# Optimization experiments

Measured on AMD Instinct MI355X. Metric: run time of the kernel, lower is better.

Reference implementation:

```python
import jax, jax.numpy as jnp
import numpy as np

N_QUBITS = 18
BATCH = 8
LAYERS = 4


def setup_inputs() -> dict:
    key = jax.random.key(0)
    k1, k2 = jax.random.split(key)
    batch_betas = jax.random.normal(k1, (BATCH, LAYERS), dtype=jnp.float32)
    adj_matrices = jax.random.uniform(k2, (BATCH, N_QUBITS, N_QUBITS), dtype=jnp.float32)
    return {"batch_betas": batch_betas, "adj_matrices": adj_matrices}


def reference(batch_betas, adj_matrices):
    B, P = batch_betas.shape
    N = adj_matrices.shape[-1]
    dim = 2 ** N

    # Z_i diagonal for qubit i: ones(2^i) kron [1,-1] kron ones(2^(N-1-i)),
    # i.e. z_i(x) = 1 - 2 * bit_{N-1-i}(x).
    idx = jnp.arange(dim)
    shifts = (N - 1 - jnp.arange(N))[:, None]
    Z = 1.0 - 2.0 * ((idx[None, :] >> shifts) & 1).astype(jnp.float32)  # [N, dim]

    # MaxCut diagonal: sum over upper-triangular edges of 0.5 * (1 - z_u * z_v)
    W = (jnp.triu(adj_matrices, k=1) > 0.5).astype(jnp.float32)  # [B, N, N]
    n_edges = jnp.sum(W, axis=(1, 2))                            # [B]
    T = jnp.einsum('buv,vd->bud', W, Z)                          # [B, N, dim]
    cross = jnp.einsum('bud,ud->bd', T, Z)                       # sum_{u<v} W z_u z_v
    hp_diag = 0.5 * (n_edges[:, None] - cross)                   # [B, dim]

    # uniform superposition
    state = jnp.full((B, dim), 1.0 / np.sqrt(dim), dtype=jnp.complex64)
    phase = jnp.exp(-1j * hp_diag)  # e^{-i * H_P * 1.0}, complex64

    for t in range(P):
        state = state * phase
        beta = batch_betas[:, t]
        c = jnp.cos(beta).astype(jnp.complex64)[:, None, None]
        ms = (-1j * jnp.sin(beta).astype(jnp.complex64))[:, None, None]
        # apply RX-like mixer [[c, -i s], [-i s, c]] to each qubit
        for i in range(N):
            s4 = state.reshape(B, 2 ** i, 2, -1)
            s0 = s4[:, :, 0, :]
            s1 = s4[:, :, 1, :]
            new0 = c * s0 + ms * s1
            new1 = ms * s0 + c * s1
            state = jnp.stack([new0, new1], axis=2).reshape(B, dim)

    probs = jnp.abs(state) ** 2
    energy = jnp.sum(probs * hp_diag, axis=1)  # [B]
    return energy
```

## Files before the change

### kernel.cpp

```cpp
#include <hip/hip_runtime.h>
#include <hip/hip_fp16.h>

#define NQ 18
#define QDIM (1 << NQ)
#define NB 8
#define NL 4

typedef unsigned u32;
typedef unsigned long long u64;

#define DPP_XOR1 0xB1
#define DPP_XOR2 0x4E

__device__ __forceinline__ void tbfly(float2& a, float2& b, float t) {
  float nax = fmaf(t, b.y, a.x);
  float nay = fmaf(-t, b.x, a.y);
  float nbx = fmaf(t, a.y, b.x);
  float nby = fmaf(-t, a.x, b.y);
  a = make_float2(nax, nay); b = make_float2(nbx, nby);
}
__device__ __forceinline__ void tstage(float2* v, int m, float t) {
#pragma unroll
  for (int i = 0; i < 16; ++i)
    if (!(i & m)) tbfly(v[i], v[i | m], t);
}
template <int CTRL>
__device__ __forceinline__ void dppstage(float2* v, float t) {
#pragma unroll
  for (int k = 0; k < 16; ++k) {
    float ox = __int_as_float(
        __builtin_amdgcn_mov_dpp(__float_as_int(v[k].x), CTRL, 0xF, 0xF, true));
    float oy = __int_as_float(
        __builtin_amdgcn_mov_dpp(__float_as_int(v[k].y), CTRL, 0xF, 0xF, true));
    v[k] = make_float2(fmaf(t, oy, v[k].x), fmaf(-t, ox, v[k].y));
  }
}
__device__ __forceinline__ void mixA(float2* v, float t) {
  tstage(v, 1, t); tstage(v, 2, t); tstage(v, 4, t); tstage(v, 8, t);
  dppstage<DPP_XOR1>(v, t); dppstage<DPP_XOR2>(v, t);
}
__device__ __forceinline__ void mixB(float2* v, float t) {
  tstage(v, 1, t); tstage(v, 2, t); tstage(v, 4, t); tstage(v, 8, t);
  dppstage<DPP_XOR1>(v, t); dppstage<DPP_XOR2>(v, t);
}
__device__ __forceinline__ void pmul(float2& a, float2 p) {
  a = make_float2(a.x * p.x - a.y * p.y, a.x * p.y + a.y * p.x);
}
__device__ __forceinline__ int swz(int byte) { return byte ^ (((byte >> 7) & 7) << 4); }

__device__ __forceinline__ float2 h2f(u32 u) {
  __half2 h; *(u32*)&h = u; return __half22float2(h);
}
__device__ __forceinline__ u32 f2h(float2 f) {
  __half2 h = __float22half2_rn(f); return *(u32*)&h;
}

template <int MODE>
__global__ __launch_bounds__(256)
void k_low(const float* __restrict__ betas, const float* __restrict__ adj,
           unsigned char* __restrict__ hp8, u32* __restrict__ state,
           float* __restrict__ out, int t0) {
  __shared__ float2 swapb[4096];
  __shared__ float2 ptab[160];
  __shared__ unsigned smask[NQ];
  __shared__ unsigned sfull[4];
  __shared__ int sdeg[4];
  __shared__ float wsum[4];

  const int tid = threadIdx.x;
  const int l = tid & 63, w = tid >> 6;
  const int b = blockIdx.x & 7;
  const int blk6 = blockIdx.x >> 3;
  const size_t bb = (size_t)b << NQ;
  const int lbase = blk6 << 12;
  char* L = (char*)swapb;
  const int leB = ((l & 3) << 6) | (w << 4) | ((l >> 2) & 15);
  const int bB  = leB << 3;

  const float beta0 = betas[b * NL + t0];
  float s0, c0; sincosf(beta0, &s0, &c0);
  const float tf0 = s0 / c0;
  const float c0p2 = c0 * c0, c0p4 = c0p2 * c0p2;
  const float c0p12 = c0p4 * c0p4 * c0p4;

  float tf1 = 0.f, scale = 1.f;
  if (MODE == 0) scale = 0.001953125f * c0p12;
  if (MODE == 1) {
    const float beta1 = betas[b * NL + t0 + 1];
    float s1, c1; sincosf(beta1, &s1, &c1);
    tf1 = s1 / c1;
    const float c1p2 = c1 * c1, c1p4 = c1p2 * c1p2;
    scale = c0p12 * (c1p4 * c1p4 * c1p4);
  }

  if (MODE == 0) {
    if (tid < NQ) {
      unsigned m = 0;
      const float* row = adj + ((size_t)b * NQ + tid) * NQ;
      for (int vq = tid + 1; vq < NQ; ++vq)
        if (row[vq] > 0.5f) m |= 1u << (NQ - 1 - vq);
      smask[tid] = m;
    }
    if (blk6 == 0 && tid == 0) out[b] = 0.f;
    __syncthreads();
    if (tid < 4) {
      unsigned fm = smask[17 - tid];
      for (int uq = 0; uq < NQ; ++uq)
        if ((smask[uq] >> tid) & 1u) fm |= 1u << (17 - uq);
      sfull[tid] = fm; sdeg[tid] = __popc(fm);
    }
  }
  if (MODE != 2 && tid < 160) {
    float ss, cc; sincosf((float)tid, &ss, &cc);
    ptab[tid] = make_float2(cc * scale, -ss * scale);
  }

  float2 v[16];

  if (MODE == 0) {
    __syncthreads();
    unsigned d = (unsigned)(lbase | (tid << 4));
    int hp = 0;
#pragma unroll
    for (int uq = 0; uq < NQ; ++uq) {
      const unsigned f = (d >> (17 - uq)) & 1u;
      hp += __popc(smask[uq] & (d ^ (0u - f)));
    }
    u64 plo = (u64)hp, phi = 0;
    int j = 0;
#pragma unroll
    for (int i = 1; i < 16; ++i) {
      const int p = __ffs(i) - 1;
      const int old = (int)((d >> p) & 1u);
      const int nb1 = __popc(sfull[p] & d);
      hp += old ? (2 * nb1 - sdeg[p]) : (sdeg[p] - 2 * nb1);
      d ^= 1u << p; j ^= 1 << p;
      if (j < 8) plo |= (u64)hp << (8 * j);
      else       phi |= (u64)hp << (8 * (j - 8));
    }
    uint4 hq;
    hq.x = (unsigned)plo; hq.y = (unsigned)(plo >> 32);
    hq.z = (unsigned)phi; hq.w = (unsigned)(phi >> 32);
    *(uint4*)(hp8 + bb + (size_t)(lbase + (tid << 4))) = hq;
#pragma unroll
    for (int jj = 0; jj < 16; ++jj) {
      const int h = (jj < 8) ? (int)((plo >> (8 * jj)) & 255)
                             : (int)((phi >> (8 * (jj - 8))) & 255);
      v[jj] = ptab[h];
    }
    mixA(v, tf0);
#pragma unroll
    for (int q = 0; q < 8; ++q)
      *(float4*)(L + swz((tid << 7) + (q << 4))) =
          make_float4(v[2*q].x, v[2*q].y, v[2*q+1].x, v[2*q+1].y);
    __syncthreads();
#pragma unroll
    for (int jj = 0; jj < 16; ++jj)
      v[jj] = *(const float2*)(L + swz((jj << 11) + bB));
    mixB(v, tf0);
#pragma unroll
    for (int jj = 0; jj < 16; ++jj)
      *(float2*)(L + swz((jj << 11) + bB)) = v[jj];
    __syncthreads();
#pragma unroll
    for (int q = 0; q < 8; ++q) {
      const float4 f = *(const float4*)(L + swz((tid << 7) + (q << 4)));
      v[2*q]   = make_float2(f.x, f.y);
      v[2*q+1] = make_float2(f.z, f.w);
    }
    uint4* gdst = (uint4*)(state + bb + lbase + (tid << 4));
#pragma unroll
    for (int q = 0; q < 4; ++q) {
      uint4 t4;
      t4.x = f2h(v[4*q]);   t4.y = f2h(v[4*q+1]);
      t4.z = f2h(v[4*q+2]); t4.w = f2h(v[4*q+3]);
      gdst[q] = t4;
    }
    return;
  }

  const uint4* gsrc = (const uint4*)(state + bb + lbase + (tid << 4));
#pragma unroll
  for (int q = 0; q < 4; ++q) {
    const uint4 t4 = gsrc[q];
    v[4*q]   = h2f(t4.x); v[4*q+1] = h2f(t4.y);
    v[4*q+2] = h2f(t4.z); v[4*q+3] = h2f(t4.w);
  }
  mixA(v, tf0);
#pragma unroll
  for (int q = 0; q < 8; ++q)
    *(float4*)(L + swz((tid << 7) + (q << 4))) =
        make_float4(v[2*q].x, v[2*q].y, v[2*q+1].x, v[2*q+1].y);
  __syncthreads();
#pragma unroll
  for (int jj = 0; jj < 16; ++jj)
    v[jj] = *(const float2*)(L + swz((jj << 11) + bB));
  mixB(v, tf0);

  if (MODE == 1) {
    const unsigned char* hq = hp8 + bb + (size_t)(lbase + leB);
#pragma unroll
    for (int jj = 0; jj < 16; ++jj)
      pmul(v[jj], ptab[hq[jj << 8]]);
    mixB(v, tf1);
#pragma unroll
    for (int jj = 0; jj < 16; ++jj)
      *(float2*)(L + swz((jj << 11) + bB)) = v[jj];
    __syncthreads();
#pragma unroll
    for (int q = 0; q < 8; ++q) {
      const float4 f = *(const float4*)(L + swz((tid << 7) + (q << 4)));
      v[2*q]   = make_float2(f.x, f.y);
      v[2*q+1] = make_float2(f.z, f.w);
    }
    mixA(v, tf1);
    uint4* gdst = (uint4*)(state + bb + lbase + (tid << 4));
#pragma unroll
    for (int q = 0; q < 4; ++q) {
      uint4 t4;
      t4.x = f2h(v[4*q]);   t4.y = f2h(v[4*q+1]);
      t4.z = f2h(v[4*q+2]); t4.w = f2h(v[4*q+3]);
      gdst[q] = t4;
    }
  } else {
    const unsigned char* hq = hp8 + bb + (size_t)(lbase + leB);
    float acc = 0.f;
#pragma unroll
    for (int jj = 0; jj < 16; ++jj) {
      const float h = (float)hq[jj << 8];
      const float wx = v[jj].x * c0p12, wy = v[jj].y * c0p12;
      acc = fmaf(wx * wx + wy * wy, h, acc);
    }
#pragma unroll
    for (int m = 1; m <= 32; m <<= 1) acc += __shfl_xor(acc, m, 64);
    if (l == 0) wsum[w] = acc;
    __syncthreads();
    if (tid == 0) atomicAdd(out + b, wsum[0] + wsum[1] + wsum[2] + wsum[3]);
  }
}

__global__ __launch_bounds__(256)
void k_high(const float* __restrict__ betas, const unsigned char* __restrict__ hp8,
            u32* __restrict__ state, int t0) {
  __shared__ float2 swapb[4096];
  __shared__ float2 ptab[160];
  const int tid = threadIdx.x;
  const int w2 = tid >> 6, lane = tid & 63;
  const int b = blockIdx.x & 7;
  const int mid = blockIdx.x >> 3;
  const size_t bb = (size_t)b << NQ;
  const int base = (mid << 6) | lane;

  const float beta0 = betas[b * NL + t0], beta1 = betas[b * NL + t0 + 1];
  float s0, c0, s1, c1;
  sincosf(beta0, &s0, &c0); sincosf(beta1, &s1, &c1);
  const float tf0 = s0 / c0, tf1 = s1 / c1;
  const float c0p2 = c0 * c0, c1p2 = c1 * c1;
  const float scale = (c0p2 * c0p2 * c0p2) * (c1p2 * c1p2 * c1p2);
  if (tid < 160) {
    float ss, cc; sincosf((float)tid, &ss, &cc);
    ptab[tid] = make_float2(cc * scale, -ss * scale);
  }

  float2 v[16];
#pragma unroll
  for (int j = 0; j < 16; ++j)
    v[j] = h2f(state[bb + ((size_t)((w2 << 4) | j) << 12) + base]);
  tstage(v, 1, tf0); tstage(v, 2, tf0); tstage(v, 4, tf0); tstage(v, 8, tf0);
#pragma unroll
  for (int j = 0; j < 16; ++j)
    swapb[(((w2 << 4) | j) << 6) | lane] = v[j];
  __syncthreads();
#pragma unroll
  for (int j = 0; j < 16; ++j)
    v[j] = swapb[(((j << 2) | w2) << 6) | lane];
  tstage(v, 4, tf0); tstage(v, 8, tf0);
#pragma unroll
  for (int j = 0; j < 16; ++j) {
    const int h = hp8[bb + ((size_t)((j << 2) | w2) << 12) + base];
    pmul(v[j], ptab[h]);
  }
  tstage(v, 4, tf1); tstage(v, 8, tf1);
#pragma unroll
  for (int j = 0; j < 16; ++j)
    swapb[(((j << 2) | w2) << 6) | lane] = v[j];
  __syncthreads();
#pragma unroll
  for (int j = 0; j < 16; ++j)
    v[j] = swapb[(((w2 << 4) | j) << 6) | lane];
  tstage(v, 1, tf1); tstage(v, 2, tf1); tstage(v, 4, tf1); tstage(v, 8, tf1);
#pragma unroll
  for (int j = 0; j < 16; ++j)
    state[bb + ((size_t)((w2 << 4) | j) << 12) + base] = f2h(v[j]);
}

extern "C" void kernel_launch(void* const* d_in, const int* in_sizes, int n_in,
                              void* d_out, int out_size, void* d_ws, size_t ws_size,
                              hipStream_t stream) {
  const float* betas = (const float*)d_in[0];
  const float* adj   = (const float*)d_in[1];
  float* out = (float*)d_out;
  char* ws = (char*)d_ws;
  u32* state = (u32*)ws;
  unsigned char* hp8 = (unsigned char*)(ws + (size_t)NB * QDIM * 4);

  dim3 grid(NB * 64), blk(256);
  k_low<0><<<grid, blk, 0, stream>>>(betas, adj, hp8, state, out, 0);
  k_high  <<<grid, blk, 0, stream>>>(betas, hp8, state, 0);
  k_low<1><<<grid, blk, 0, stream>>>(betas, adj, hp8, state, out, 1);
  k_high  <<<grid, blk, 0, stream>>>(betas, hp8, state, 2);
  k_low<2><<<grid, blk, 0, stream>>>(betas, adj, hp8, state, out, 3);
}
```

Before: 41.91 us.

## Use 512-thread blocks with 8 elements per thread and restructured qubit split

Doubles the threads per block to 512 and halves the per-thread register tile from 16 to 8 amplitudes. The per-thread qubit decomposition is reorganized into three in-register stages, two DPP stages and a cross-half-wave shuffle stage, with a new LDS transpose index mapping. The aim is more parallelism and latency hiding with lower register pressure. In exchange each thread does less work between barriers, and the xor-32 shuffle is likely costlier than DPP.

```diff
diff --git a/kernel.cpp b/kernel.cpp
--- a/kernel.cpp
+++ b/kernel.cpp
@@ -19,15 +19,15 @@
   float nby = fmaf(-t, a.x, b.y);
   a = make_float2(nax, nay); b = make_float2(nbx, nby);
 }
-__device__ __forceinline__ void tstage(float2* v, int m, float t) {
-#pragma unroll
-  for (int i = 0; i < 16; ++i)
+__device__ __forceinline__ void tstage8(float2* v, int m, float t) {
+#pragma unroll
+  for (int i = 0; i < 8; ++i)
     if (!(i & m)) tbfly(v[i], v[i | m], t);
 }
 template <int CTRL>
-__device__ __forceinline__ void dppstage(float2* v, float t) {
-#pragma unroll
-  for (int k = 0; k < 16; ++k) {
+__device__ __forceinline__ void dppstage8(float2* v, float t) {
+#pragma unroll
+  for (int k = 0; k < 8; ++k) {
     float ox = __int_as_float(
         __builtin_amdgcn_mov_dpp(__float_as_int(v[k].x), CTRL, 0xF, 0xF, true));
     float oy = __int_as_float(
@@ -35,13 +35,18 @@
     v[k] = make_float2(fmaf(t, oy, v[k].x), fmaf(-t, ox, v[k].y));
   }
 }
-__device__ __forceinline__ void mixA(float2* v, float t) {
-  tstage(v, 1, t); tstage(v, 2, t); tstage(v, 4, t); tstage(v, 8, t);
-  dppstage<DPP_XOR1>(v, t); dppstage<DPP_XOR2>(v, t);
-}
-__device__ __forceinline__ void mixB(float2* v, float t) {
-  tstage(v, 1, t); tstage(v, 2, t); tstage(v, 4, t); tstage(v, 8, t);
-  dppstage<DPP_XOR1>(v, t); dppstage<DPP_XOR2>(v, t);
+__device__ __forceinline__ void shfl32stage8(float2* v, float t) {
+#pragma unroll
+  for (int k = 0; k < 8; ++k) {
+    float ox = __shfl_xor(v[k].x, 32, 64);
+    float oy = __shfl_xor(v[k].y, 32, 64);
+    v[k] = make_float2(fmaf(t, oy, v[k].x), fmaf(-t, ox, v[k].y));
+  }
+}
+__device__ __forceinline__ void mix6(float2* v, float t) {
+  tstage8(v, 1, t); tstage8(v, 2, t); tstage8(v, 4, t);
+  dppstage8<DPP_XOR1>(v, t); dppstage8<DPP_XOR2>(v, t);
+  shfl32stage8(v, t);
 }
 __device__ __forceinline__ void pmul(float2& a, float2 p) {
   a = make_float2(a.x * p.x - a.y * p.y, a.x * p.y + a.y * p.x);
@@ -56,16 +61,16 @@
 }
 
 template <int MODE>
-__global__ __launch_bounds__(256)
+__global__ __launch_bounds__(512)
 void k_low(const float* __restrict__ betas, const float* __restrict__ adj,
            unsigned char* __restrict__ hp8, u32* __restrict__ state,
            float* __restrict__ out, int t0) {
   __shared__ float2 swapb[4096];
   __shared__ float2 ptab[160];
   __shared__ unsigned smask[NQ];
-  __shared__ unsigned sfull[4];
-  __shared__ int sdeg[4];
-  __shared__ float wsum[4];
+  __shared__ unsigned sfull[3];
+  __shared__ int sdeg[3];
+  __shared__ float wsum[8];
 
   const int tid = threadIdx.x;
   const int l = tid & 63, w = tid >> 6;
@@ -74,8 +79,9 @@
   const size_t bb = (size_t)b << NQ;
   const int lbase = blk6 << 12;
   char* L = (char*)swapb;
-  const int leB = ((l & 3) << 6) | (w << 4) | ((l >> 2) & 15);
-  const int bB  = leB << 3;
+  const int constB = ((w >> 2) << 8) | (((l >> 5) & 1) << 7) | (((l >> 1) & 1) << 6)
+                   | ((l & 1) << 5) | ((w & 3) << 3) | ((l >> 2) & 7);
+  const int bBbase = constB << 3;
 
   const float beta0 = betas[b * NL + t0];
   float s0, c0; sincosf(beta0, &s0, &c0);
@@ -102,132 +108,120 @@
       smask[tid] = m;
     }
     if (blk6 == 0 && tid == 0) out[b] = 0.f;
-    __syncthreads();
-    if (tid < 4) {
+    if (tid < 160) {
+      float ss, cc; sincosf((float)tid, &ss, &cc);
+      ptab[tid] = make_float2(cc * scale, -ss * scale);
+    }
+    __syncthreads();
+    if (tid < 3) {
       unsigned fm = smask[17 - tid];
       for (int uq = 0; uq < NQ; ++uq)
         if ((smask[uq] >> tid) & 1u) fm |= 1u << (17 - uq);
       sfull[tid] = fm; sdeg[tid] = __popc(fm);
     }
-  }
-  if (MODE != 2 && tid < 160) {
-    float ss, cc; sincosf((float)tid, &ss, &cc);
-    ptab[tid] = make_float2(cc * scale, -ss * scale);
-  }
-
-  float2 v[16];
+    __syncthreads();
+  } else if (MODE == 1) {
+    if (tid < 160) {
+      float ss, cc; sincosf((float)tid, &ss, &cc);
+      ptab[tid] = make_float2(cc * scale, -ss * scale);
+    }
+    __syncthreads();
+  }
+
+  float2 v[8];
 
   if (MODE == 0) {
-    __syncthreads();
-    unsigned d = (unsigned)(lbase | (tid << 4));
+    unsigned d = (unsigned)(lbase | (tid << 3));
     int hp = 0;
 #pragma unroll
     for (int uq = 0; uq < NQ; ++uq) {
       const unsigned f = (d >> (17 - uq)) & 1u;
       hp += __popc(smask[uq] & (d ^ (0u - f)));
     }
-    u64 plo = (u64)hp, phi = 0;
+    u64 pk = (u64)hp;
     int j = 0;
 #pragma unroll
-    for (int i = 1; i < 16; ++i) {
+    for (int i = 1; i < 8; ++i) {
       const int p = __ffs(i) - 1;
       const int old = (int)((d >> p) & 1u);
       const int nb1 = __popc(sfull[p] & d);
       hp += old ? (2 * nb1 - sdeg[p]) : (sdeg[p] - 2 * nb1);
       d ^= 1u << p; j ^= 1 << p;
-      if (j < 8) plo |= (u64)hp << (8 * j);
-      else       phi |= (u64)hp << (8 * (j - 8));
-    }
-    uint4 hq;
-    hq.x = (unsigned)plo; hq.y = (unsigned)(plo >> 32);
-    hq.z = (unsigned)phi; hq.w = (unsigned)(phi >> 32);
-    *(uint4*)(hp8 + bb + (size_t)(lbase + (tid << 4))) = hq;
-#pragma unroll
-    for (int jj = 0; jj < 16; ++jj) {
-      const int h = (jj < 8) ? (int)((plo >> (8 * jj)) & 255)
-                             : (int)((phi >> (8 * (jj - 8))) & 255);
-      v[jj] = ptab[h];
-    }
-    mixA(v, tf0);
-#pragma unroll
-    for (int q = 0; q < 8; ++q)
-      *(float4*)(L + swz((tid << 7) + (q << 4))) =
+      pk |= (u64)hp << (8 * j);
+    }
+    *(u64*)(hp8 + bb + (size_t)(lbase + (tid << 3))) = pk;
+#pragma unroll
+    for (int jj = 0; jj < 8; ++jj)
+      v[jj] = ptab[(int)((pk >> (8 * jj)) & 255)];
+    mix6(v, tf0);
+#pragma unroll
+    for (int q = 0; q < 4; ++q)
+      *(float4*)(L + swz((tid << 6) | (q << 4))) =
           make_float4(v[2*q].x, v[2*q].y, v[2*q+1].x, v[2*q+1].y);
     __syncthreads();
 #pragma unroll
-    for (int jj = 0; jj < 16; ++jj)
-      v[jj] = *(const float2*)(L + swz((jj << 11) + bB));
-    mixB(v, tf0);
-#pragma unroll
-    for (int jj = 0; jj < 16; ++jj)
-      *(float2*)(L + swz((jj << 11) + bB)) = v[jj];
-    __syncthreads();
-#pragma unroll
-    for (int q = 0; q < 8; ++q) {
-      const float4 f = *(const float4*)(L + swz((tid << 7) + (q << 4)));
+    for (int jj = 0; jj < 8; ++jj)
+      v[jj] = *(const float2*)(L + swz((jj << 12) + bBbase));
+    mix6(v, tf0);
+#pragma unroll
+    for (int jj = 0; jj < 8; ++jj)
+      *(float2*)(L + swz((jj << 12) + bBbase)) = v[jj];
+    __syncthreads();
+#pragma unroll
+    for (int q = 0; q < 4; ++q) {
+      const float4 f = *(const float4*)(L + swz((tid << 6) | (q << 4)));
       v[2*q]   = make_float2(f.x, f.y);
       v[2*q+1] = make_float2(f.z, f.w);
     }
-    uint4* gdst = (uint4*)(state + bb + lbase + (tid << 4));
-#pragma unroll
-    for (int q = 0; q < 4; ++q) {
-      uint4 t4;
-      t4.x = f2h(v[4*q]);   t4.y = f2h(v[4*q+1]);
-      t4.z = f2h(v[4*q+2]); t4.w = f2h(v[4*q+3]);
-      gdst[q] = t4;
-    }
+    uint4* gdst = (uint4*)(state + bb + lbase + (tid << 3));
+    gdst[0] = make_uint4(f2h(v[0]), f2h(v[1]), f2h(v[2]), f2h(v[3]));
+    gdst[1] = make_uint4(f2h(v[4]), f2h(v[5]), f2h(v[6]), f2h(v[7]));
     return;
   }
 
-  const uint4* gsrc = (const uint4*)(state + bb + lbase + (tid << 4));
-#pragma unroll
-  for (int q = 0; q < 4; ++q) {
-    const uint4 t4 = gsrc[q];
-    v[4*q]   = h2f(t4.x); v[4*q+1] = h2f(t4.y);
-    v[4*q+2] = h2f(t4.z); v[4*q+3] = h2f(t4.w);
-  }
-  mixA(v, tf0);
-#pragma unroll
-  for (int q = 0; q < 8; ++q)
-    *(float4*)(L + swz((tid << 7) + (q << 4))) =
+  const uint4* gsrc = (const uint4*)(state + bb + lbase + (tid << 3));
+  {
+    const uint4 t4a = gsrc[0], t4b = gsrc[1];
+    v[0] = h2f(t4a.x); v[1] = h2f(t4a.y); v[2] = h2f(t4a.z); v[3] = h2f(t4a.w);
+    v[4] = h2f(t4b.x); v[5] = h2f(t4b.y); v[6] = h2f(t4b.z); v[7] = h2f(t4b.w);
+  }
+  mix6(v, tf0);
+#pragma unroll
+  for (int q = 0; q < 4; ++q)
+    *(float4*)(L + swz((tid << 6) | (q << 4))) =
         make_float4(v[2*q].x, v[2*q].y, v[2*q+1].x, v[2*q+1].y);
   __syncthreads();
 #pragma unroll
-  for (int jj = 0; jj < 16; ++jj)
-    v[jj] = *(const float2*)(L + swz((jj << 11) + bB));
-  mixB(v, tf0);
+  for (int jj = 0; jj < 8; ++jj)
+    v[jj] = *(const float2*)(L + swz((jj << 12) + bBbase));
+  mix6(v, tf0);
 
   if (MODE == 1) {
-    const unsigned char* hq = hp8 + bb + (size_t)(lbase + leB);
-#pragma unroll
-    for (int jj = 0; jj < 16; ++jj)
-      pmul(v[jj], ptab[hq[jj << 8]]);
-    mixB(v, tf1);
-#pragma unroll
-    for (int jj = 0; jj < 16; ++jj)
-      *(float2*)(L + swz((jj << 11) + bB)) = v[jj];
-    __syncthreads();
-#pragma unroll
-    for (int q = 0; q < 8; ++q) {
-      const float4 f = *(const float4*)(L + swz((tid << 7) + (q << 4)));
+    const unsigned char* hq = hp8 + bb + (size_t)(lbase + constB);
+#pragma unroll
+    for (int jj = 0; jj < 8; ++jj)
+      pmul(v[jj], ptab[hq[jj << 9]]);
+    mix6(v, tf1);
+#pragma unroll
+    for (int jj = 0; jj < 8; ++jj)
+      *(float2*)(L + swz((jj << 12) + bBbase)) = v[jj];
+    __syncthreads();
+#pragma unroll
+    for (int q = 0; q < 4; ++q) {
+      const float4 f = *(const float4*)(L + swz((tid << 6) | (q << 4)));
       v[2*q]   = make_float2(f.x, f.y);
       v[2*q+1] = make_float2(f.z, f.w);
     }
-    mixA(v, tf1);
-    uint4* gdst = (uint4*)(state + bb + lbase + (tid << 4));
-#pragma unroll
-    for (int q = 0; q < 4; ++q) {
-      uint4 t4;
-      t4.x = f2h(v[4*q]);   t4.y = f2h(v[4*q+1]);
-      t4.z = f2h(v[4*q+2]); t4.w = f2h(v[4*q+3]);
-      gdst[q] = t4;
-    }
+    mix6(v, tf1);
+    uint4* gdst = (uint4*)(state + bb + lbase + (tid << 3));
+    gdst[0] = make_uint4(f2h(v[0]), f2h(v[1]), f2h(v[2]), f2h(v[3]));
+    gdst[1] = make_uint4(f2h(v[4]), f2h(v[5]), f2h(v[6]), f2h(v[7]));
   } else {
-    const unsigned char* hq = hp8 + bb + (size_t)(lbase + leB);
+    const unsigned char* hq = hp8 + bb + (size_t)(lbase + constB);
     float acc = 0.f;
 #pragma unroll
-    for (int jj = 0; jj < 16; ++jj) {
-      const float h = (float)hq[jj << 8];
+    for (int jj = 0; jj < 8; ++jj) {
+      const float h = (float)hq[jj << 9];
       const float wx = v[jj].x * c0p12, wy = v[jj].y * c0p12;
       acc = fmaf(wx * wx + wy * wy, h, acc);
     }
@@ -235,21 +229,26 @@
     for (int m = 1; m <= 32; m <<= 1) acc += __shfl_xor(acc, m, 64);
     if (l == 0) wsum[w] = acc;
     __syncthreads();
-    if (tid == 0) atomicAdd(out + b, wsum[0] + wsum[1] + wsum[2] + wsum[3]);
-  }
-}
-
-__global__ __launch_bounds__(256)
+    if (tid == 0) {
+      float s = 0.f;
+#pragma unroll
+      for (int i = 0; i < 8; ++i) s += wsum[i];
+      atomicAdd(out + b, s);
+    }
+  }
+}
+
+__global__ __launch_bounds__(512)
 void k_high(const float* __restrict__ betas, const unsigned char* __restrict__ hp8,
             u32* __restrict__ state, int t0) {
   __shared__ float2 swapb[4096];
   __shared__ float2 ptab[160];
   const int tid = threadIdx.x;
-  const int w2 = tid >> 6, lane = tid & 63;
+  const int col = tid & 63, w = tid >> 6;
   const int b = blockIdx.x & 7;
   const int mid = blockIdx.x >> 3;
   const size_t bb = (size_t)b << NQ;
-  const int base = (mid << 6) | lane;
+  const int cbase = (mid << 6) | col;
 
   const float beta0 = betas[b * NL + t0], beta1 = betas[b * NL + t0 + 1];
   float s0, c0, s1, c1;
@@ -261,37 +260,38 @@
     float ss, cc; sincosf((float)tid, &ss, &cc);
     ptab[tid] = make_float2(cc * scale, -ss * scale);
   }
-
-  float2 v[16];
-#pragma unroll
-  for (int j = 0; j < 16; ++j)
-    v[j] = h2f(state[bb + ((size_t)((w2 << 4) | j) << 12) + base]);
-  tstage(v, 1, tf0); tstage(v, 2, tf0); tstage(v, 4, tf0); tstage(v, 8, tf0);
-#pragma unroll
-  for (int j = 0; j < 16; ++j)
-    swapb[(((w2 << 4) | j) << 6) | lane] = v[j];
   __syncthreads();
-#pragma unroll
-  for (int j = 0; j < 16; ++j)
-    v[j] = swapb[(((j << 2) | w2) << 6) | lane];
-  tstage(v, 4, tf0); tstage(v, 8, tf0);
-#pragma unroll
-  for (int j = 0; j < 16; ++j) {
-    const int h = hp8[bb + ((size_t)((j << 2) | w2) << 12) + base];
+
+  float2 v[8];
+#pragma unroll
+  for (int j = 0; j < 8; ++j)
+    v[j] = h2f(state[bb + ((size_t)((w << 3) | j) << 12) + cbase]);
+  tstage8(v, 1, tf0); tstage8(v, 2, tf0); tstage8(v, 4, tf0);
+#pragma unroll
+  for (int j = 0; j < 8; ++j)
+    swapb[(((w << 3) | j) << 6) | col] = v[j];
+  __syncthreads();
+#pragma unroll
+  for (int j = 0; j < 8; ++j)
+    v[j] = swapb[(((j << 3) | w) << 6) | col];
+  tstage8(v, 1, tf0); tstage8(v, 2, tf0); tstage8(v, 4, tf0);
+#pragma unroll
+  for (int j = 0; j < 8; ++j) {
+    const int h = hp8[bb + ((size_t)((j << 3) | w) << 12) + cbase];
     pmul(v[j], ptab[h]);
   }
-  tstage(v, 4, tf1); tstage(v, 8, tf1);
-#pragma unroll
-  for (int j = 0; j < 16; ++j)
-    swapb[(((j << 2) | w2) << 6) | lane] = v[j];
+  tstage8(v, 1, tf1); tstage8(v, 2, tf1); tstage8(v, 4, tf1);
+#pragma unroll
+  for (int j = 0; j < 8; ++j)
+    swapb[(((j << 3) | w) << 6) | col] = v[j];
   __syncthreads();
 #pragma unroll
-  for (int j = 0; j < 16; ++j)
-    v[j] = swapb[(((w2 << 4) | j) << 6) | lane];
-  tstage(v, 1, tf1); tstage(v, 2, tf1); tstage(v, 4, tf1); tstage(v, 8, tf1);
-#pragma unroll
-  for (int j = 0; j < 16; ++j)
-    state[bb + ((size_t)((w2 << 4) | j) << 12) + base] = f2h(v[j]);
+  for (int j = 0; j < 8; ++j)
+    v[j] = swapb[(((w << 3) | j) << 6) | col];
+  tstage8(v, 1, tf1); tstage8(v, 2, tf1); tstage8(v, 4, tf1);
+#pragma unroll
+  for (int j = 0; j < 8; ++j)
+    state[bb + ((size_t)((w << 3) | j) << 12) + cbase] = f2h(v[j]);
 }
 
 extern "C" void kernel_launch(void* const* d_in, const int* in_sizes, int n_in,
@@ -304,7 +304,7 @@
   u32* state = (u32*)ws;
   unsigned char* hp8 = (unsigned char*)(ws + (size_t)NB * QDIM * 4);
 
-  dim3 grid(NB * 64), blk(256);
+  dim3 grid(NB * 64), blk(512);
   k_low<0><<<grid, blk, 0, stream>>>(betas, adj, hp8, state, out, 0);
   k_high  <<<grid, blk, 0, stream>>>(betas, hp8, state, 0);
   k_low<1><<<grid, blk, 0, stream>>>(betas, adj, hp8, state, out, 1);
```

After: 41.42 us. Within noise of the previous version (-1.2%).
